# Optimization experiments

Hardware: AMD Instinct MI355X
Metric: run time of the kernel (lower is better)

The kernel has to match this reference:

```python
import jax, jax.numpy as jnp
import numpy as np

B, L, H, V = 32, 4096, 512, 32000


def setup_inputs() -> dict:
    key = jax.random.key(0)
    ks = jax.random.split(key, 16)
    s = 0.02  # weight init scale
    return {
        "input_token": jax.random.normal(ks[0], (B, H), jnp.float32),
        "h0": jax.random.normal(ks[1], (B, H), jnp.float32),
        "c0": jax.random.normal(ks[2], (B, H), jnp.float32),
        "document_output": jax.random.normal(ks[3], (B, L, H), jnp.float32),
        "document_mask": jax.random.randint(ks[4], (B, L), 0, 2, jnp.int32),
        "W_ih": jax.random.normal(ks[5], (4 * H, H), jnp.float32) * s,
        "W_hh": jax.random.normal(ks[6], (4 * H, H), jnp.float32) * s,
        "b_ih": jax.random.normal(ks[7], (4 * H,), jnp.float32) * s,
        "b_hh": jax.random.normal(ks[8], (4 * H,), jnp.float32) * s,
        "W1_w": jax.random.normal(ks[9], (H, H), jnp.float32) * s,
        "W1_b": jax.random.normal(ks[10], (H,), jnp.float32) * s,
        "W2_w": jax.random.normal(ks[11], (H, H), jnp.float32) * s,
        "W2_b": jax.random.normal(ks[12], (H,), jnp.float32) * s,
        "u1": jax.random.normal(ks[13], (H,), jnp.float32),
        "Wout_w": jax.random.normal(ks[14], (V, 2 * H), jnp.float32) * s,
        "Wout_b": jax.random.normal(ks[15], (V,), jnp.float32) * s,
    }


def reference(input_token, h0, c0, document_output, document_mask,
              W_ih, W_hh, b_ih, b_hh, W1_w, W1_b, W2_w, W2_b, u1,
              Wout_w, Wout_b):
    # Single LSTM step (torch gate order: i, f, g, o)
    gates = input_token @ W_ih.T + b_ih + h0 @ W_hh.T + b_hh  # (B, 4H)
    i, f, g, o = jnp.split(gates, 4, axis=-1)
    c = jax.nn.sigmoid(f) * c0 + jax.nn.sigmoid(i) * jnp.tanh(g)
    h = jax.nn.sigmoid(o) * jnp.tanh(c)  # (B, H)

    # Additive (Bahdanau) attention over document positions
    q = h @ W1_w.T + W1_b                                     # (B, H)
    k = document_output @ W2_w.T + W2_b                       # (B, L, H)
    combined = jnp.tanh(q[:, None, :] + k)                    # (B, L, H)
    scores = jnp.einsum("blh,h->bl", combined, u1)            # (B, L)
    scores = jnp.where(document_mask.astype(bool), scores, -jnp.inf)
    attn = jax.nn.softmax(scores, axis=1)                     # (B, L)
    context = jnp.einsum("bl,blh->bh", attn, document_output)  # (B, H)

    combined_context = jnp.concatenate([h, context], axis=1)  # (B, 2H)
    output = combined_context @ Wout_w.T + Wout_b             # (B, V)
    return output, h, c
```

## Files before the change

kernel.cpp:

```cpp
#include <hip/hip_runtime.h>
#include <hip/hip_bf16.h>
#include <math.h>

#define B_  32
#define L_  4096
#define H_  512
#define V_  32000
#define MBLK 128

typedef __attribute__((ext_vector_type(4))) float f32x4;
typedef __attribute__((ext_vector_type(2))) float f32x2;
typedef __attribute__((ext_vector_type(8))) short short8;
typedef __attribute__((ext_vector_type(4))) unsigned short u16x4;

__device__ __forceinline__ unsigned short bf16_rne(float x){
  union { float f; unsigned int u; } v; v.f = x;
  unsigned int u = v.u;
  return (unsigned short)((u + 0x7FFFu + ((u >> 16) & 1u)) >> 16);
}
__device__ __forceinline__ float bf16_f32(unsigned short h){
  union { unsigned int u; float f; } v; v.u = ((unsigned int)h) << 16;
  return v.f;
}
__device__ __forceinline__ float tanh_cheap(float x){
  float e = __expf(x + x);
  return 1.0f - 2.0f * __builtin_amdgcn_rcpf(e + 1.0f);
}
__device__ __forceinline__ short8 cvt8(f32x4 a, f32x4 b){
  union { __hip_bfloat162 h[4]; short8 s; } u;
  u.h[0] = __float22bfloat162_rn(make_float2(a[0], a[1]));
  u.h[1] = __float22bfloat162_rn(make_float2(a[2], a[3]));
  u.h[2] = __float22bfloat162_rn(make_float2(b[0], b[1]));
  u.h[3] = __float22bfloat162_rn(make_float2(b[2], b[3]));
  return u.s;
}

__global__ __launch_bounds__(256) void k_convert_w2(
    const float* __restrict__ w2, unsigned short* __restrict__ w2t){
  int idx = blockIdx.x * 256 + threadIdx.x;
  int j = idx & 511, kc = idx >> 9;
  const float* src = w2 + j*512 + kc*8;
  f32x4 a = *(const f32x4*)src;
  f32x4 b = *(const f32x4*)(src + 4);
  *(short8*)(w2t + (long)(kc*512 + j)*8) = cvt8(a, b);
}

__global__ __launch_bounds__(256) void k_gates(
    const float* __restrict__ x, const float* __restrict__ h0,
    const float* __restrict__ Wih, const float* __restrict__ Whh,
    const float* __restrict__ bih, const float* __restrict__ bhh,
    float* __restrict__ gates){
  __shared__ float sx[H_], sh[H_];
  int b = blockIdx.y, t = threadIdx.x;
  sx[t] = x[b*H_ + t]; sx[t+256] = x[b*H_ + t + 256];
  sh[t] = h0[b*H_ + t]; sh[t+256] = h0[b*H_ + t + 256];
  __syncthreads();
  int j = blockIdx.x * 256 + t;
  const float* wi = Wih + j*H_;
  const float* wh = Whh + j*H_;
  float acc = bih[j] + bhh[j];
  #pragma unroll 4
  for (int k = 0; k < H_; k += 4) {
    f32x4 a = *(const f32x4*)(wi + k);
    f32x4 c = *(const f32x4*)(wh + k);
    acc += a[0]*sx[k] + a[1]*sx[k+1] + a[2]*sx[k+2] + a[3]*sx[k+3];
    acc += c[0]*sh[k] + c[1]*sh[k+1] + c[2]*sh[k+2] + c[3]*sh[k+3];
  }
  gates[b*2048 + j] = acc;
}

__global__ __launch_bounds__(256) void k_lstm(
    const float* __restrict__ gates, const float* __restrict__ c0,
    float* __restrict__ out_h, float* __restrict__ out_c, float* __restrict__ cc,
    unsigned short* __restrict__ ccb){
  int idx = blockIdx.x * 256 + threadIdx.x;
  int b = idx >> 9, hh = idx & 511;
  const float* g = gates + b*2048;
  float gi = g[hh], gf = g[512+hh], gg = g[1024+hh], go = g[1536+hh];
  float si = 1.f/(1.f+expf(-gi));
  float sf = 1.f/(1.f+expf(-gf));
  float so = 1.f/(1.f+expf(-go));
  float c = sf * c0[idx] + si * tanhf(gg);
  float h = so * tanhf(c);
  out_h[idx] = h; out_c[idx] = c;
  cc[b*1024 + hh] = h;
  ccb[b*1024 + hh] = bf16_rne(h);
}

__global__ __launch_bounds__(256) void k_q(
    const float* __restrict__ cc, const float* __restrict__ W1,
    const float* __restrict__ b1, float* __restrict__ q){
  __shared__ float shh[H_];
  int b = blockIdx.y, t = threadIdx.x;
  shh[t] = cc[b*1024 + t]; shh[t+256] = cc[b*1024 + t + 256];
  __syncthreads();
  int j = blockIdx.x*256 + t;
  const float* w = W1 + j*H_;
  float acc = b1[j];
  #pragma unroll 4
  for (int k = 0; k < H_; k += 4){
    f32x4 a = *(const f32x4*)(w + k);
    acc += a[0]*shh[k] + a[1]*shh[k+1] + a[2]*shh[k+2] + a[3]*shh[k+3];
  }
  q[b*H_ + j] = acc;
}

__global__ __launch_bounds__(512, 2) void k_scores_ctx(
    const float* __restrict__ doc, const unsigned short* __restrict__ w2t,
    const float* __restrict__ qv,
    const float* __restrict__ w2b, const float* __restrict__ u1,
    const int* __restrict__ mask,
    float* __restrict__ ctxp, float* __restrict__ bm, float* __restrict__ bs){
  __shared__ short Adoc[8][MBLK][8][8];
  __shared__ float2 s_qu[512];
  __shared__ float s_part[8][MBLK];
  __shared__ float e_arr[MBLK];
  __shared__ float wred[4];
  __shared__ float cpart[2][512];
  int t = threadIdx.x;
  int row0 = blockIdx.x * MBLK;
  int b = row0 >> 12;
  s_qu[t] = make_float2(qv[b*512 + t] + w2b[t], u1[t]);

  int sr = t >> 2;
  int sg = t & 3;
  const float* dbase = doc + (((long)(row0 + sr)) << 9) + sg*16;
  int wc0 = (2*sg)     ^ (sr & 7);
  int wc1 = (2*sg + 1) ^ (sr & 7);

  int wave = t >> 6, lane = t & 63;
  int lrow = lane & 15, lk = lane >> 4;
  int sw = lrow & 7;
  int j0 = wave * 64;
  const unsigned short* pbh = w2t + (long)(lk*512 + j0 + lrow)*8;

  f32x4 acc[8][4];
  #pragma unroll
  for (int mt = 0; mt < 8; ++mt)
    #pragma unroll
    for (int jj = 0; jj < 4; ++jj)
      acc[mt][jj] = (f32x4){0.f, 0.f, 0.f, 0.f};

  {
    f32x4 v0 = *(const f32x4*)(dbase);
    f32x4 v1 = *(const f32x4*)(dbase + 4);
    f32x4 v2 = *(const f32x4*)(dbase + 8);
    f32x4 v3 = *(const f32x4*)(dbase + 12);
    *(short8*)&Adoc[0][sr][wc0][0] = cvt8(v0, v1);
    *(short8*)&Adoc[0][sr][wc1][0] = cvt8(v2, v3);
  }
  __syncthreads();

  for (int s = 0; s < 8; ++s){
    short8 bh[8];
    {
      const unsigned short* pb = pbh + (long)s*8*512*8;
      #pragma unroll
      for (int jj = 0; jj < 4; ++jj){
        bh[jj]   = *(const short8*)(pb + jj*128);
        bh[4+jj] = *(const short8*)(pb + 4*512*8 + jj*128);
      }
    }
    f32x4 pf0, pf1, pf2, pf3;
    if (s < 7){
      const float* p = dbase + (s+1)*64;
      pf0 = *(const f32x4*)(p);
      pf1 = *(const f32x4*)(p + 4);
      pf2 = *(const f32x4*)(p + 8);
      pf3 = *(const f32x4*)(p + 12);
    }
    #pragma unroll
    for (int ktl = 0; ktl < 2; ++ktl){
      short8 a[8];
      #pragma unroll
      for (int mt = 0; mt < 8; ++mt)
        a[mt] = *(const short8*)&Adoc[s][mt*16 + lrow][(ktl*4 + lk) ^ sw][0];
      #pragma unroll
      for (int jj = 0; jj < 4; ++jj)
        #pragma unroll
        for (int mt = 0; mt < 8; ++mt)
          acc[mt][jj] = __builtin_amdgcn_mfma_f32_16x16x32_bf16(bh[ktl*4 + jj], a[mt], acc[mt][jj], 0, 0, 0);
    }
    if (s < 7){
      *(short8*)&Adoc[s+1][sr][wc0][0] = cvt8(pf0, pf1);
      *(short8*)&Adoc[s+1][sr][wc1][0] = cvt8(pf2, pf3);
    }
    __syncthreads();
  }

  #pragma unroll
  for (int mt = 0; mt < 8; ++mt){
    float p = 0.f;
    #pragma unroll
    for (int jj = 0; jj < 4; ++jj){
      #pragma unroll
      for (int r = 0; r < 4; ++r){
        int j = j0 + jj*16 + lk*4 + r;
        float2 qu = s_qu[j];
        p += tanh_cheap(acc[mt][jj][r] + qu.x) * qu.y;
      }
    }
    p += __shfl_xor(p, 16);
    p += __shfl_xor(p, 32);
    if (lane < 16) s_part[wave][mt*16 + lrow] = p;
  }
  __syncthreads();

  float sl = 0.f;
  bool ok = false;
  if (t < MBLK){
    #pragma unroll
    for (int w = 0; w < 8; ++w) sl += s_part[w][t];
    ok = mask[row0 + t] != 0;
    sl = ok ? sl : -INFINITY;
    float m = sl;
    #pragma unroll
    for (int o = 1; o < 64; o <<= 1) m = fmaxf(m, __shfl_xor(m, o));
    if (lane == 0) wred[wave] = m;
  }
  __syncthreads();
  if (t < MBLK){
    float mb = fmaxf(wred[0], wred[1]);
    float e = ok ? __expf(sl - mb) : 0.f;
    float es = e;
    #pragma unroll
    for (int o = 1; o < 64; o <<= 1) es += __shfl_xor(es, o);
    if (lane == 0) wred[2 + wave] = es;
    e_arr[t] = e;
    if (t == 0) bm[blockIdx.x] = mb;
  }
  __syncthreads();
  if (t == 0) bs[blockIdx.x] = wred[2] + wred[3];

  {
    int p = t & 255, half = t >> 8;
    int h0 = 2*p;
    int sstep = h0 >> 6;
    int c = (h0 >> 3) & 7;
    int e = h0 & 7;
    float a0 = 0.f, a1 = 0.f;
    int l0 = half * 64;
    #pragma unroll 8
    for (int l = l0; l < l0 + 64; ++l){
      int cp = c ^ (l & 7);
      unsigned v = *(const unsigned*)((const char*)&Adoc[sstep][l][cp][0] + e*2);
      float el = e_arr[l];
      a0 += el * bf16_f32((unsigned short)(v & 0xffff));
      a1 += el * bf16_f32((unsigned short)(v >> 16));
    }
    cpart[half][2*p]   = a0;
    cpart[half][2*p+1] = a1;
  }
  __syncthreads();
  ctxp[(long)blockIdx.x * 512 + t] = cpart[0][t] + cpart[1][t];
}

__global__ __launch_bounds__(512) void k_combine(
    const float* __restrict__ ctxp, const float* __restrict__ bm,
    const float* __restrict__ bs, unsigned short* __restrict__ ccb){
  __shared__ float sw[32];
  __shared__ float sT;
  int b = blockIdx.x, t = threadIdx.x;
  if (t < 32){
    float m = bm[b*32 + t], s = bs[b*32 + t];
    float M = m;
    #pragma unroll
    for (int o = 1; o < 32; o <<= 1) M = fmaxf(M, __shfl_xor(M, o));
    float w = (m == -INFINITY) ? 0.f : __expf(m - M);
    float ts = s * w;
    #pragma unroll
    for (int o = 1; o < 32; o <<= 1) ts += __shfl_xor(ts, o);
    sw[t] = w;
    if (t == 0) sT = ts;
  }
  __syncthreads();
  float invT = 1.f / sT;
  const float* cp = ctxp + (long)b*32*512 + t;
  float acc = 0.f;
  #pragma unroll 8
  for (int blk = 0; blk < 32; ++blk) acc += cp[blk*512] * sw[blk];
  ccb[b*1024 + 512 + t] = bf16_rne(acc * invT);
}

__global__ __launch_bounds__(512, 2) void k_out(
    const unsigned short* __restrict__ ccb, const float* __restrict__ Wout,
    const float* __restrict__ bout, float* __restrict__ out){
  __shared__ short Ccb[32][128][8];
  int t = threadIdx.x, wave = t >> 6, lane = t & 63;
  int v0 = blockIdx.x * 128;
  #pragma unroll
  for (int i = 0; i < 8; ++i){
    int c16 = i*512 + t;
    int bb = c16 >> 7, ch = c16 & 127;
    int chsw = (ch & ~7) | ((ch & 7) ^ (bb & 7));
    *(short8*)&Ccb[bb][chsw][0] = *(const short8*)(ccb + c16*8);
  }
  __syncthreads();

  int lrow = lane & 15, lk = lane >> 4;
  int vrow = v0 + wave*16 + lrow;
  const float* wptr = Wout + (long)vrow*1024 + lk*8;
  f32x4 acc[2];
  acc[0] = (f32x4){0.f,0.f,0.f,0.f};
  acc[1] = (f32x4){0.f,0.f,0.f,0.f};
  int sw = lrow & 7;
  f32x4 w0 = *(const f32x4*)(wptr);
  f32x4 w1 = *(const f32x4*)(wptr + 4);
  #pragma unroll 4
  for (int ks = 0; ks < 32; ++ks){
    f32x4 nw0, nw1;
    if (ks < 31){
      nw0 = *(const f32x4*)(wptr + (ks+1)*32);
      nw1 = *(const f32x4*)(wptr + (ks+1)*32 + 4);
    }
    short8 bfrag = cvt8(w0, w1);
    int ch = ks*4 + lk;
    int chsw = (ch & ~7) | ((ch & 7) ^ sw);
    short8 a0 = *(const short8*)&Ccb[lrow][chsw][0];
    short8 a1 = *(const short8*)&Ccb[16 + lrow][chsw][0];
    acc[0] = __builtin_amdgcn_mfma_f32_16x16x32_bf16(bfrag, a0, acc[0], 0, 0, 0);
    acc[1] = __builtin_amdgcn_mfma_f32_16x16x32_bf16(bfrag, a1, acc[1], 0, 0, 0);
    w0 = nw0; w1 = nw1;
  }
  int vcol = v0 + wave*16 + lk*4;
  f32x4 bo4 = *(const f32x4*)&bout[vcol];
  #pragma unroll
  for (int mt = 0; mt < 2; ++mt){
    f32x4 res;
    res[0] = acc[mt][0] + bo4[0];
    res[1] = acc[mt][1] + bo4[1];
    res[2] = acc[mt][2] + bo4[2];
    res[3] = acc[mt][3] + bo4[3];
    *(f32x4*)&out[(long)(mt*16 + lrow)*V_ + vcol] = res;
  }
}

extern "C" void kernel_launch(void* const* d_in, const int* in_sizes, int n_in,
                              void* d_out, int out_size, void* d_ws, size_t ws_size,
                              hipStream_t stream){
  const float* x    = (const float*)d_in[0];
  const float* h0   = (const float*)d_in[1];
  const float* c0   = (const float*)d_in[2];
  const float* doc  = (const float*)d_in[3];
  const int*   mask = (const int*)d_in[4];
  const float* Wih  = (const float*)d_in[5];
  const float* Whh  = (const float*)d_in[6];
  const float* bih  = (const float*)d_in[7];
  const float* bhh  = (const float*)d_in[8];
  const float* W1   = (const float*)d_in[9];
  const float* b1   = (const float*)d_in[10];
  const float* W2   = (const float*)d_in[11];
  const float* b2   = (const float*)d_in[12];
  const float* u1   = (const float*)d_in[13];
  const float* Wo   = (const float*)d_in[14];
  const float* bo   = (const float*)d_in[15];
  float* out  = (float*)d_out;
  float* outh = out + B_*V_;
  float* outc = outh + B_*H_;

  float* ws    = (float*)d_ws;
  float* gates = ws;
  float* q     = gates + 65536;
  float* cc    = q + 16384;
  float* ctxp  = cc + 32768;
  float* bm    = ctxp + 524288;
  float* bs    = bm + 1024;
  unsigned short* w2t = (unsigned short*)(bs + 1024);
  unsigned short* ccb = w2t + 262144;

  hipLaunchKernelGGL(k_convert_w2, dim3(128), dim3(256), 0, stream, W2, w2t);
  hipLaunchKernelGGL(k_gates, dim3(8, 32), dim3(256), 0, stream, x, h0, Wih, Whh, bih, bhh, gates);
  hipLaunchKernelGGL(k_lstm, dim3(64), dim3(256), 0, stream, gates, c0, outh, outc, cc, ccb);
  hipLaunchKernelGGL(k_q, dim3(2, 32), dim3(256), 0, stream, cc, W1, b1, q);
  hipLaunchKernelGGL(k_scores_ctx, dim3(1024), dim3(512), 0, stream, doc, w2t, q, b2, u1, mask, ctxp, bm, bs);
  hipLaunchKernelGGL(k_combine, dim3(32), dim3(512), 0, stream, ctxp, bm, bs, ccb);
  hipLaunchKernelGGL(k_out, dim3(250), dim3(512), 0, stream, ccb, Wo, bo, out);
}
```

Measured before the change: 225.9 us.

## Preload full doc tile into LDS upfront, add MFMA priority, shrink k_out blocks

The scores kernel now loads and converts all eight K-slices of the document tile into shared memory before a single barrier, instead of double-buffering one slice ahead with a barrier per step. This removes the seven per-step barriers but issues all global loads up front, so they no longer overlap with the MFMAs. s_setprio raises wave priority around the MFMA bursts. The output GEMM kernel moves to 256-thread blocks covering 64 vocab rows each, doubling the grid to 500 blocks, which also doubles how often the shared ccb tile is reloaded.

Result: faster. 215.7 us (-4.5%).

```diff
diff --git a/kernel.cpp b/kernel.cpp
--- a/kernel.cpp
+++ b/kernel.cpp
@@ -141,16 +141,19 @@
     for (int jj = 0; jj < 4; ++jj)
       acc[mt][jj] = (f32x4){0.f, 0.f, 0.f, 0.f};
 
-  {
-    f32x4 v0 = *(const f32x4*)(dbase);
-    f32x4 v1 = *(const f32x4*)(dbase + 4);
-    f32x4 v2 = *(const f32x4*)(dbase + 8);
-    f32x4 v3 = *(const f32x4*)(dbase + 12);
-    *(short8*)&Adoc[0][sr][wc0][0] = cvt8(v0, v1);
-    *(short8*)&Adoc[0][sr][wc1][0] = cvt8(v2, v3);
-  }
-  __syncthreads();
-
+  #pragma unroll
+  for (int slot = 0; slot < 8; ++slot){
+    const float* p = dbase + slot*64;
+    f32x4 v0 = *(const f32x4*)(p);
+    f32x4 v1 = *(const f32x4*)(p + 4);
+    f32x4 v2 = *(const f32x4*)(p + 8);
+    f32x4 v3 = *(const f32x4*)(p + 12);
+    *(short8*)&Adoc[slot][sr][wc0][0] = cvt8(v0, v1);
+    *(short8*)&Adoc[slot][sr][wc1][0] = cvt8(v2, v3);
+  }
+  __syncthreads();
+
+  #pragma unroll 1
   for (int s = 0; s < 8; ++s){
     short8 bh[8];
     {
@@ -161,31 +164,21 @@
         bh[4+jj] = *(const short8*)(pb + 4*512*8 + jj*128);
       }
     }
-    f32x4 pf0, pf1, pf2, pf3;
-    if (s < 7){
-      const float* p = dbase + (s+1)*64;
-      pf0 = *(const f32x4*)(p);
-      pf1 = *(const f32x4*)(p + 4);
-      pf2 = *(const f32x4*)(p + 8);
-      pf3 = *(const f32x4*)(p + 12);
-    }
     #pragma unroll
     for (int ktl = 0; ktl < 2; ++ktl){
       short8 a[8];
       #pragma unroll
       for (int mt = 0; mt < 8; ++mt)
         a[mt] = *(const short8*)&Adoc[s][mt*16 + lrow][(ktl*4 + lk) ^ sw][0];
+      __builtin_amdgcn_s_setprio(1);
       #pragma unroll
       for (int jj = 0; jj < 4; ++jj)
         #pragma unroll
         for (int mt = 0; mt < 8; ++mt)
-          acc[mt][jj] = __builtin_amdgcn_mfma_f32_16x16x32_bf16(bh[ktl*4 + jj], a[mt], acc[mt][jj], 0, 0, 0);
-    }
-    if (s < 7){
-      *(short8*)&Adoc[s+1][sr][wc0][0] = cvt8(pf0, pf1);
-      *(short8*)&Adoc[s+1][sr][wc1][0] = cvt8(pf2, pf3);
-    }
-    __syncthreads();
+          acc[mt][jj] = __builtin_amdgcn_mfma_f32_16x16x32_bf16(
+              bh[ktl*4 + jj], a[mt], acc[mt][jj], 0, 0, 0);
+      __builtin_amdgcn_s_setprio(0);
+    }
   }
 
   #pragma unroll
@@ -282,15 +275,15 @@
   ccb[b*1024 + 512 + t] = bf16_rne(acc * invT);
 }
 
-__global__ __launch_bounds__(512, 2) void k_out(
+__global__ __launch_bounds__(256, 2) void k_out(
     const unsigned short* __restrict__ ccb, const float* __restrict__ Wout,
     const float* __restrict__ bout, float* __restrict__ out){
   __shared__ short Ccb[32][128][8];
   int t = threadIdx.x, wave = t >> 6, lane = t & 63;
-  int v0 = blockIdx.x * 128;
-  #pragma unroll
-  for (int i = 0; i < 8; ++i){
-    int c16 = i*512 + t;
+  int v0 = blockIdx.x * 64;
+  #pragma unroll
+  for (int i = 0; i < 16; ++i){
+    int c16 = i*256 + t;
     int bb = c16 >> 7, ch = c16 & 127;
     int chsw = (ch & ~7) | ((ch & 7) ^ (bb & 7));
     *(short8*)&Ccb[bb][chsw][0] = *(const short8*)(ccb + c16*8);
@@ -374,5 +367,5 @@
   hipLaunchKernelGGL(k_q, dim3(2, 32), dim3(256), 0, stream, cc, W1, b1, q);
   hipLaunchKernelGGL(k_scores_ctx, dim3(1024), dim3(512), 0, stream, doc, w2t, q, b2, u1, mask, ctxp, bm, bs);
   hipLaunchKernelGGL(k_combine, dim3(32), dim3(512), 0, stream, ctxp, bm, bs, ccb);
-  hipLaunchKernelGGL(k_out, dim3(250), dim3(512), 0, stream, ccb, Wo, bo, out);
-}
+  hipLaunchKernelGGL(k_out, dim3(500), dim3(256), 0, stream, ccb, Wo, bo, out);
+}
```
